# Kernel optimization log

Hardware: AMD Instinct MI355X
Metric: run time of the kernel (lower is better)

## Reference

```python
import jax
import jax.numpy as jnp
import numpy as np

B, N, C_IN, C_OUT, K = 16, 4096, 64, 128, 16
RATIO = 0.25
M = int(RATIO * N)  # 1024 sampled points per cloud
EPS = 1e-5


def setup_inputs() -> dict:
    key = jax.random.key(0)
    ks = jax.random.split(key, 4)
    features = jax.random.normal(ks[0], (B, N, C_IN), dtype=jnp.float32)
    positions = jax.random.normal(ks[1], (B, N, 3), dtype=jnp.float32)
    batch = jnp.repeat(jnp.arange(B, dtype=jnp.int64), N)  # [B*N]
    W = jax.random.normal(ks[2], (C_IN, C_OUT), dtype=jnp.float32) * 0.1
    b = jax.random.normal(ks[3], (C_OUT,), dtype=jnp.float32) * 0.1
    gamma = jnp.ones((C_OUT,), dtype=jnp.float32)
    beta = jnp.zeros((C_OUT,), dtype=jnp.float32)
    return {"features": features, "positions": positions, "batch": batch,
            "W": W, "b": b, "gamma": gamma, "beta": beta}


def _fps_single(pos):
    """Farthest point sampling on one cloud. pos: [N,3] -> indices [M] (start at 0)."""
    def step(carry, _):
        min_d, last = carry
        d = jnp.sum((pos - pos[last]) ** 2, axis=-1)       # [N]
        min_d = jnp.minimum(min_d, d)
        nxt = jnp.argmax(min_d).astype(jnp.int32)
        return (min_d, nxt), nxt
    init = (jnp.full((N,), 1e10, dtype=pos.dtype), jnp.int32(0))
    _, rest = jax.lax.scan(step, init, None, length=M - 1)
    return jnp.concatenate([jnp.zeros((1,), jnp.int32), rest])


def reference(features, positions, batch, W, b, gamma, beta):
    # --- FPS per batch (on positions) ---
    fps_idx = jax.vmap(_fps_single)(positions)                     # [B, M] int32

    # --- MLP: Linear + BatchNorm1d (training-mode batch stats over all B*N points) ---
    h = jnp.einsum('bnc,co->bno', features, W) + b                 # [B, N, C_OUT]
    flat = h.reshape(-1, C_OUT)
    mean = jnp.mean(flat, axis=0)
    var = jnp.mean((flat - mean) ** 2, axis=0)                     # biased, as BN
    hn = (h - mean) * jax.lax.rsqrt(var + EPS) * gamma + beta      # [B, N, C_OUT]

    # --- kNN in FEATURE space: queries = sampled features, keys = all features ---
    q = jnp.take_along_axis(features, fps_idx[..., None], axis=1)  # [B, M, C_IN]
    d2 = (jnp.sum(q * q, -1)[:, :, None]
          + jnp.sum(features * features, -1)[:, None, :]
          - 2.0 * jnp.einsum('bmd,bnd->bmn', q, features))         # [B, M, N]
    _, nbr = jax.lax.top_k(-d2, K)                                 # [B, M, K]

    # --- gather MLP'd features at neighbors, max-pool per sampled point ---
    gathered = jnp.take_along_axis(hn, nbr.reshape(B, M * K)[..., None], axis=1)
    new_features = gathered.reshape(B, M, K, C_OUT).max(axis=2)    # [B, M, C_OUT]

    new_positions = jnp.take_along_axis(positions, fps_idx[..., None], axis=1)  # [B, M, 3]
    new_batch = jnp.take_along_axis(batch.reshape(B, N), fps_idx.astype(jnp.int64), axis=1).reshape(-1)
    return new_features, new_positions, new_batch
```

## Files before the change

kernel.cpp:

```cpp
#include <hip/hip_runtime.h>

#define B_ 16
#define N_ 4096
#define CIN_ 64
#define COUT_ 128
#define K_ 16
#define M_ 1024

typedef float f32x2 __attribute__((ext_vector_type(2)));
typedef unsigned long long u64;

#define DPPF(m, ctrl)                                                          \
  m = fmaxf(m, __int_as_float(__builtin_amdgcn_update_dpp(                     \
                  0, __float_as_int(m), ctrl, 0xF, 0xF, true)))
#define DPPI(e, ctrl)                                                          \
  e = max(e, __builtin_amdgcn_update_dpp(0, e, ctrl, 0xF, 0xF, true))

__device__ __forceinline__ unsigned mono32(float d) {
  unsigned u = __float_as_uint(d);
  return u ^ (unsigned)(((int)u >> 31) | 0x80000000);
}

__global__ __launch_bounds__(512) void mega_kernel(
    const float* __restrict__ pos, const float* __restrict__ features,
    const float* __restrict__ W, const float* __restrict__ bias,
    int* __restrict__ fps_idx, float* __restrict__ h,
    float* __restrict__ stats, int* __restrict__ prog,
    u64* __restrict__ cand, int S) {
  __shared__ __align__(16) char smem[84 * 1024];
  const int id = blockIdx.x;
  const int t = threadIdx.x;

  if (id < B_) {
    const int b = id;
    float4* P = (float4*)smem;
    u64* red = (u64*)(smem + 65536);
    const float* pb = pos + (size_t)b * N_ * 3;
    for (int i = t; i < N_; i += 512)
      P[i] = make_float4(pb[i * 3], pb[i * 3 + 1], pb[i * 3 + 2], 0.f);
    __syncthreads();
    if (t < 256) {
      f32x2 px[8], py[8], pz[8], md[8];
#pragma unroll
      for (int j = 0; j < 8; ++j) {
        const float4 lo = P[t + 512 * j];
        const float4 hi = P[t + 512 * j + 256];
        px[j] = (f32x2){lo.x, hi.x};
        py[j] = (f32x2){lo.y, hi.y};
        pz[j] = (f32x2){lo.z, hi.z};
        md[j] = (f32x2){1e10f, 1e10f};
      }
      if (t == 0) fps_idx[b * M_] = 0;
      const int wv = t >> 6, ln = t & 63;
      const int e0 = 65535 - t;
      float4 lp = P[0];
      for (int step = 1; step < M_; ++step) {
        const f32x2 lx = {lp.x, lp.x}, ly = {lp.y, lp.y}, lz = {lp.z, lp.z};
        float bestd = -1.0f;
        int be = 0;
        {
#pragma clang fp contract(off)
#pragma unroll
          for (int j = 0; j < 8; ++j) {
            const f32x2 dx = px[j] - lx;
            const f32x2 dy = py[j] - ly;
            const f32x2 dz = pz[j] - lz;
            const f32x2 s1 = dx * dx;
            const f32x2 s2 = dy * dy;
            const f32x2 s3 = dz * dz;
            const f32x2 d = (s1 + s2) + s3;
            f32x2 nd;
            nd.x = fminf(md[j].x, d.x);
            nd.y = fminf(md[j].y, d.y);
            md[j] = nd;
            if (nd.x > bestd) { bestd = nd.x; be = e0 - (j << 9); }
            if (nd.y > bestd) { bestd = nd.y; be = e0 - (j << 9) - 256; }
          }
        }
        float m = bestd;
        DPPF(m, 0x111); DPPF(m, 0x112); DPPF(m, 0x114); DPPF(m, 0x118);
        DPPF(m, 0x142); DPPF(m, 0x143);
        const float wm =
            __int_as_float(__builtin_amdgcn_readlane(__float_as_int(m), 63));
        int enc = (bestd == wm) ? be : 0;
        DPPI(enc, 0x111); DPPI(enc, 0x112); DPPI(enc, 0x114); DPPI(enc, 0x118);
        DPPI(enc, 0x142); DPPI(enc, 0x143);
        const int wenc = __builtin_amdgcn_readlane(enc, 63);
        if (ln == 0)
          red[(step & 1) * 4 + wv] =
              ((u64)__float_as_uint(wm) << 32) | (unsigned)wenc;
        __syncthreads();
        const u64* rb = &red[(step & 1) * 4];
        u64 rr = rb[0] > rb[1] ? rb[0] : rb[1];
        const u64 r2 = rb[2] > rb[3] ? rb[2] : rb[3];
        if (r2 > rr) rr = r2;
        const int last = 65535 - (int)(unsigned)(rr & 0xFFFFFFFFu);
        lp = P[last];
        if (t == 0) {
          fps_idx[b * M_ + step] = last;
          if ((step & 63) == 63)
            __hip_atomic_store(&prog[b], (step >> 6) + 1, __ATOMIC_RELEASE,
                               __HIP_MEMORY_SCOPE_AGENT);
        }
      }
    } else {
      for (int step = 1; step < M_; ++step) __syncthreads();
    }
    return;
  }

  if (id < B_ + 256 * S) {
    const int kid = id - B_;
    const int qt = kid / (B_ * S);
    const int rem = kid % (B_ * S);
    const int b = rem / S;
    const int s = rem % S;
    const int KPS = N_ / S;
    const int KT = KPS / 128;
    float* Qs = (float*)smem;
    float* Ks = (float*)(smem + 16384);
    float* sd2 = (float*)(smem + 49152);
    float* qq = (float*)(smem + 82944);
    float* ff = (float*)(smem + 83200);
    int* qid = (int*)(smem + 83712);
    const float* fb = features + (size_t)b * N_ * CIN_;

    if (t == 0) {
      while (__hip_atomic_load(&prog[b], __ATOMIC_ACQUIRE,
                               __HIP_MEMORY_SCOPE_AGENT) < qt + 1)
        __builtin_amdgcn_s_sleep(16);
    }
    __syncthreads();
    if (t < 64) qid[t] = fps_idx[b * M_ + qt * 64 + t];
    __syncthreads();
#pragma unroll
    for (int st = 0; st < 2; ++st) {
      const int iid = t + 512 * st;
      const int row = iid >> 4, c4 = iid & 15;
      const int pc = (c4 + (row >> 2)) & 15;
      const float4 v = *(const float4*)(fb + (size_t)qid[row] * CIN_ + c4 * 4);
      *(float4*)(&Qs[row * 64 + pc * 4]) = v;
    }
    __syncthreads();
    if (t < 64) {
      float sv = 0.f;
#pragma unroll
      for (int c4 = 0; c4 < 16; ++c4) {
        const int pc = (c4 + (t >> 2)) & 15;
        const float4 v = *(const float4*)(&Qs[t * 64 + pc * 4]);
        sv = fmaf(v.x, v.x, sv); sv = fmaf(v.y, v.y, sv);
        sv = fmaf(v.z, v.z, sv); sv = fmaf(v.w, v.w, sv);
      }
      qq[t] = sv;
    }

    u64 lst[16];
#pragma unroll
    for (int p = 0; p < 16; ++p) lst[p] = ~0ull;
    u64 worst = ~0ull;
    int wpos = 0;

    const int q0 = (t >> 5) * 4;
    const int k0 = (t & 31) * 4;
    const int sq = t >> 3;
    const int ssub = t & 7;

    for (int kt = 0; kt < KT; ++kt) {
      const int kb = s * KPS + kt * 128;
#pragma unroll
      for (int st = 0; st < 4; ++st) {
        const int iid = t + 512 * st;
        const int row = iid >> 4, c4 = iid & 15;
        const int pc = (c4 + (row >> 2)) & 15;
        const float4 v = *(const float4*)(fb + (size_t)(kb + row) * CIN_ + c4 * 4);
        *(float4*)(&Ks[row * 64 + pc * 4]) = v;
      }
      __syncthreads();
      if (t < 128) {
        float sv = 0.f;
#pragma unroll
        for (int c4 = 0; c4 < 16; ++c4) {
          const int pc = (c4 + (t >> 2)) & 15;
          const float4 v = *(const float4*)(&Ks[t * 64 + pc * 4]);
          sv = fmaf(v.x, v.x, sv); sv = fmaf(v.y, v.y, sv);
          sv = fmaf(v.z, v.z, sv); sv = fmaf(v.w, v.w, sv);
        }
        ff[t] = sv;
      }
      __syncthreads();
      float acc[4][4];
#pragma unroll
      for (int i = 0; i < 4; ++i)
#pragma unroll
        for (int j = 0; j < 4; ++j) acc[i][j] = 0.f;
#pragma unroll
      for (int c4 = 0; c4 < 16; ++c4) {
        float4 qv[4], kv[4];
#pragma unroll
        for (int i = 0; i < 4; ++i) {
          const int row = q0 + i;
          const int pc = (c4 + (row >> 2)) & 15;
          qv[i] = *(const float4*)(&Qs[row * 64 + pc * 4]);
        }
#pragma unroll
        for (int j = 0; j < 4; ++j) {
          const int row = k0 + j;
          const int pc = (c4 + (row >> 2)) & 15;
          kv[j] = *(const float4*)(&Ks[row * 64 + pc * 4]);
        }
#pragma unroll
        for (int i = 0; i < 4; ++i)
#pragma unroll
          for (int j = 0; j < 4; ++j) {
            acc[i][j] = fmaf(qv[i].x, kv[j].x, acc[i][j]);
            acc[i][j] = fmaf(qv[i].y, kv[j].y, acc[i][j]);
            acc[i][j] = fmaf(qv[i].z, kv[j].z, acc[i][j]);
            acc[i][j] = fmaf(qv[i].w, kv[j].w, acc[i][j]);
          }
      }
#pragma unroll
      for (int i = 0; i < 4; ++i) {
        const float qv = qq[q0 + i];
        float4 o;
        o.x = __fsub_rn(__fadd_rn(qv, ff[k0 + 0]), 2.f * acc[i][0]);
        o.y = __fsub_rn(__fadd_rn(qv, ff[k0 + 1]), 2.f * acc[i][1]);
        o.z = __fsub_rn(__fadd_rn(qv, ff[k0 + 2]), 2.f * acc[i][2]);
        o.w = __fsub_rn(__fadd_rn(qv, ff[k0 + 3]), 2.f * acc[i][3]);
        *(float4*)(&sd2[(q0 + i) * 132 + k0]) = o;
      }
      __syncthreads();
#pragma unroll
      for (int g = 0; g < 4; ++g) {
        const float4 v = *(const float4*)(&sd2[sq * 132 + ssub * 16 + g * 4]);
        const float dv[4] = {v.x, v.y, v.z, v.w};
#pragma unroll
        for (int jj = 0; jj < 4; ++jj) {
          const int key = kb + ssub * 16 + g * 4 + jj;
          const u64 pk = ((u64)mono32(dv[jj]) << 32) | (unsigned)key;
          if (pk < worst) {
#pragma unroll
            for (int p = 0; p < 16; ++p)
              if (p == wpos) lst[p] = pk;
            worst = lst[0]; wpos = 0;
#pragma unroll
            for (int p = 1; p < 16; ++p)
              if (lst[p] > worst) { worst = lst[p]; wpos = p; }
          }
        }
      }
      __syncthreads();
    }
    u64* cb = cand + ((size_t)(b * M_ + qt * 64 + sq) * S + s) * 16;
    for (int r = 0; r < K_; ++r) {
      u64 mn = lst[0];
#pragma unroll
      for (int p = 1; p < 16; ++p)
        if (lst[p] < mn) mn = lst[p];
      u64 m2 = mn;
#pragma unroll
      for (int off = 1; off < 8; off <<= 1) {
        const u64 o = __shfl_xor(m2, off, 64);
        if (o < m2) m2 = o;
      }
      if (mn == m2) {
        bool done = false;
#pragma unroll
        for (int p = 0; p < 16; ++p)
          if (!done && lst[p] == m2) { lst[p] = ~0ull; done = true; }
      }
      if (ssub == 0) cb[r] = m2;
    }
    return;
  }

  const int lid = id - (B_ + 256 * S);
  float* ls = (float*)smem;
  for (int i = t; i < 256; i += 512) ls[i] = 0.f;
  __syncthreads();
  const int o4 = (t & 31) << 2;
  const int rl = t >> 5;
  const float4 bv = *(const float4*)(bias + o4);
  float4 s4 = {0, 0, 0, 0}, ss4 = {0, 0, 0, 0};
  for (int i = 0; i < 8; ++i) {
    const int r = lid * 128 + rl * 8 + i;
    const float4* fr = (const float4*)(features + (size_t)r * CIN_);
    float4 acc = bv;
#pragma unroll
    for (int c4 = 0; c4 < 16; ++c4) {
      const float4 fv = fr[c4];
      const float* wr = W + (size_t)(c4 * 4) * COUT_ + o4;
      const float4 w0 = *(const float4*)(wr);
      const float4 w1 = *(const float4*)(wr + COUT_);
      const float4 w2 = *(const float4*)(wr + 2 * COUT_);
      const float4 w3 = *(const float4*)(wr + 3 * COUT_);
      acc.x = fmaf(fv.x, w0.x, acc.x); acc.y = fmaf(fv.x, w0.y, acc.y);
      acc.z = fmaf(fv.x, w0.z, acc.z); acc.w = fmaf(fv.x, w0.w, acc.w);
      acc.x = fmaf(fv.y, w1.x, acc.x); acc.y = fmaf(fv.y, w1.y, acc.y);
      acc.z = fmaf(fv.y, w1.z, acc.z); acc.w = fmaf(fv.y, w1.w, acc.w);
      acc.x = fmaf(fv.z, w2.x, acc.x); acc.y = fmaf(fv.z, w2.y, acc.y);
      acc.z = fmaf(fv.z, w2.z, acc.z); acc.w = fmaf(fv.z, w2.w, acc.w);
      acc.x = fmaf(fv.w, w3.x, acc.x); acc.y = fmaf(fv.w, w3.y, acc.y);
      acc.z = fmaf(fv.w, w3.z, acc.z); acc.w = fmaf(fv.w, w3.w, acc.w);
    }
    *(float4*)(h + (size_t)r * COUT_ + o4) = acc;
    s4.x += acc.x; s4.y += acc.y; s4.z += acc.z; s4.w += acc.w;
    ss4.x = fmaf(acc.x, acc.x, ss4.x); ss4.y = fmaf(acc.y, acc.y, ss4.y);
    ss4.z = fmaf(acc.z, acc.z, ss4.z); ss4.w = fmaf(acc.w, acc.w, ss4.w);
  }
  atomicAdd(&ls[o4 + 0], s4.x); atomicAdd(&ls[o4 + 1], s4.y);
  atomicAdd(&ls[o4 + 2], s4.z); atomicAdd(&ls[o4 + 3], s4.w);
  atomicAdd(&ls[128 + o4 + 0], ss4.x); atomicAdd(&ls[128 + o4 + 1], ss4.y);
  atomicAdd(&ls[128 + o4 + 2], ss4.z); atomicAdd(&ls[128 + o4 + 3], ss4.w);
  __syncthreads();
  if (t < 128) {
    atomicAdd(&stats[t], ls[t]);
    atomicAdd(&stats[128 + t], ls[128 + t]);
  }
}

__global__ void finalize_kernel(float* __restrict__ stats,
                                const float* __restrict__ gamma,
                                const float* __restrict__ beta) {
  const int o = threadIdx.x;
  const float inv = 1.0f / (float)(B_ * N_);
  const float mean = stats[o] * inv;
  const float var = stats[128 + o] * inv - mean * mean;
  const float r = 1.0f / sqrtf(var + 1e-5f);
  const float sc = gamma[o] * r;
  stats[256 + o] = sc;
  stats[384 + o] = beta[o] - mean * sc;
}

__global__ __launch_bounds__(256) void gather_kernel(
    const float* __restrict__ h, const float* __restrict__ stats,
    const u64* __restrict__ cand, float* __restrict__ out, int S) {
  const int g = blockIdx.x;
  const int t = threadIdx.x;
  const int S16 = S * 16;
  __shared__ u64 cl[2][128];
  __shared__ int nbi[32];
  const int Q0 = g * 2;
  if (t < 2 * S16) {
    const int qi = t / S16, sl = t % S16;
    cl[qi][sl] = cand[(size_t)(Q0 + qi) * S16 + sl];
  }
  __syncthreads();
  if ((t & 127) == 0) {
    const int qi = t >> 7;
    int ptr[8] = {0, 0, 0, 0, 0, 0, 0, 0};
    for (int r = 0; r < K_; ++r) {
      u64 mn = ~0ull;
      int ms = 0;
      for (int s = 0; s < S; ++s) {
        if (ptr[s] < 16) {
          const u64 v = cl[qi][s * 16 + ptr[s]];
          if (v < mn) { mn = v; ms = s; }
        }
      }
      nbi[qi * 16 + r] = (int)(unsigned)(mn & 0xFFFFFFFFu);
      ptr[ms]++;
    }
  }
  __syncthreads();
  const int q2 = t >> 7, o = t & 127;
  const int Q = Q0 + q2, b = Q >> 10;
  const float sc = stats[256 + o];
  const float sh = stats[384 + o];
  float mx = -3.402823466e38f;
#pragma unroll
  for (int k = 0; k < K_; ++k) {
    const int n = nbi[q2 * 16 + k];
    const float v = fmaf(h[((size_t)b * N_ + n) * COUT_ + o], sc, sh);
    mx = fmaxf(mx, v);
  }
  out[(size_t)Q * COUT_ + o] = mx;
}

__global__ __launch_bounds__(256) void tail_kernel(const float* __restrict__ pos,
                                                   const int* __restrict__ fps_idx,
                                                   float* __restrict__ out,
                                                   int batch_as_i64) {
  const int gid = blockIdx.x * 256 + threadIdx.x;
  const int A = B_ * M_ * COUT_;
  const int P = B_ * M_ * 3;
  if (gid < P) {
    const int Q = gid / 3;
    const int c = gid - Q * 3;
    const int b = Q >> 10;
    const int idx = fps_idx[Q];
    out[A + gid] = pos[((size_t)b * N_ + idx) * 3 + c];
  } else {
    const int Q = gid - P;
    if (Q < B_ * M_) {
      const int b = Q >> 10;
      float* base = out + A + P;
      if (batch_as_i64)
        ((long long*)base)[Q] = (long long)b;
      else
        base[Q] = (float)b;
    }
  }
}

extern "C" void kernel_launch(void* const* d_in, const int* in_sizes, int n_in,
                              void* d_out, int out_size, void* d_ws, size_t ws_size,
                              hipStream_t stream) {
  const float* features = (const float*)d_in[0];
  const float* positions = (const float*)d_in[1];
  const float* W = (const float*)d_in[3];
  const float* bias = (const float*)d_in[4];
  const float* gamma = (const float*)d_in[5];
  const float* beta = (const float*)d_in[6];
  float* out = (float*)d_out;
  unsigned char* ws = (unsigned char*)d_ws;

  int* fps_idx = (int*)ws;
  float* h = (float*)(ws + 65536);
  const size_t hoff = 65536 + (size_t)B_ * N_ * COUT_ * 4;
  float* stats = (float*)(ws + hoff);
  int* prog = (int*)(ws + hoff + 2048);
  u64* cand = (u64*)(ws + hoff + 2048 + 256);
  const size_t base = hoff + 2048 + 256;

  int S = 8;
  while (S > 1 && base + (size_t)B_ * M_ * S * 16 * 8 > ws_size) S >>= 1;

  const int rem = out_size - (B_ * M_ * COUT_) - (B_ * M_ * 3);
  const int batch_as_i64 = (rem >= 2 * B_ * M_) ? 1 : 0;

  hipMemsetAsync(stats, 0, 2048 + 256, stream);
  mega_kernel<<<B_ + 256 * S + 512, 512, 0, stream>>>(
      positions, features, W, bias, fps_idx, h, stats, prog, cand, S);
  finalize_kernel<<<1, 128, 0, stream>>>(stats, gamma, beta);
  gather_kernel<<<B_ * M_ / 2, 256, 0, stream>>>(h, stats, cand, out, S);
  tail_kernel<<<256, 256, 0, stream>>>(positions, fps_idx, out, batch_as_i64);
}
```

Measured before the change: 1.021 ms.

## Replace FPS barrier with tagged LDS spin, store h as bf16, reorder blocks

The FPS loop's per-step __syncthreads is replaced by a lock-free handoff: each wave writes its packed max plus a step tag into double-buffered LDS, and all waves spin until every slot carries the current tag. The idle upper half of the FPS block now exits early. The MLP blocks are moved ahead of the kNN blocks in the grid so they get scheduled before the spinning kNN consumers. The intermediate h is stored as bf16 to halve its write and gather traffic, which costs precision in the gathered max-pooled outputs.

```diff
diff --git a/kernel.cpp b/kernel.cpp
--- a/kernel.cpp
+++ b/kernel.cpp
@@ -21,10 +21,18 @@
   return u ^ (unsigned)(((int)u >> 31) | 0x80000000);
 }
 
+__device__ __forceinline__ unsigned short f2bf(float x) {
+  const unsigned u = __float_as_uint(x);
+  return (unsigned short)((u + 0x7FFF + ((u >> 16) & 1)) >> 16);
+}
+__device__ __forceinline__ float bf2f(unsigned short s) {
+  return __uint_as_float((unsigned)s << 16);
+}
+
 __global__ __launch_bounds__(512) void mega_kernel(
     const float* __restrict__ pos, const float* __restrict__ features,
     const float* __restrict__ W, const float* __restrict__ bias,
-    int* __restrict__ fps_idx, float* __restrict__ h,
+    int* __restrict__ fps_idx, unsigned short* __restrict__ h,
     float* __restrict__ stats, int* __restrict__ prog,
     u64* __restrict__ cand, int S) {
   __shared__ __align__(16) char smem[84 * 1024];
@@ -34,83 +42,136 @@
   if (id < B_) {
     const int b = id;
     float4* P = (float4*)smem;
-    u64* red = (u64*)(smem + 65536);
+    volatile u64* red = (volatile u64*)(smem + 65536);
     const float* pb = pos + (size_t)b * N_ * 3;
+    if (t < 8) ((u64*)(smem + 65536))[t] = 0;
     for (int i = t; i < N_; i += 512)
       P[i] = make_float4(pb[i * 3], pb[i * 3 + 1], pb[i * 3 + 2], 0.f);
     __syncthreads();
-    if (t < 256) {
-      f32x2 px[8], py[8], pz[8], md[8];
-#pragma unroll
-      for (int j = 0; j < 8; ++j) {
-        const float4 lo = P[t + 512 * j];
-        const float4 hi = P[t + 512 * j + 256];
-        px[j] = (f32x2){lo.x, hi.x};
-        py[j] = (f32x2){lo.y, hi.y};
-        pz[j] = (f32x2){lo.z, hi.z};
-        md[j] = (f32x2){1e10f, 1e10f};
-      }
-      if (t == 0) fps_idx[b * M_] = 0;
-      const int wv = t >> 6, ln = t & 63;
-      const int e0 = 65535 - t;
-      float4 lp = P[0];
-      for (int step = 1; step < M_; ++step) {
-        const f32x2 lx = {lp.x, lp.x}, ly = {lp.y, lp.y}, lz = {lp.z, lp.z};
-        float bestd = -1.0f;
-        int be = 0;
-        {
+    if (t >= 256) return;
+    f32x2 px[8], py[8], pz[8], md[8];
+#pragma unroll
+    for (int j = 0; j < 8; ++j) {
+      const float4 lo = P[t + 512 * j];
+      const float4 hi = P[t + 512 * j + 256];
+      px[j] = (f32x2){lo.x, hi.x};
+      py[j] = (f32x2){lo.y, hi.y};
+      pz[j] = (f32x2){lo.z, hi.z};
+      md[j] = (f32x2){1e10f, 1e10f};
+    }
+    if (t == 0) fps_idx[b * M_] = 0;
+    const int wv = t >> 6, ln = t & 63;
+    const int e0 = 65535 - t;
+    float4 lp = P[0];
+    for (int step = 1; step < M_; ++step) {
+      const f32x2 lx = {lp.x, lp.x}, ly = {lp.y, lp.y}, lz = {lp.z, lp.z};
+      float bestd = -1.0f;
+      int be = 0;
+      {
 #pragma clang fp contract(off)
 #pragma unroll
-          for (int j = 0; j < 8; ++j) {
-            const f32x2 dx = px[j] - lx;
-            const f32x2 dy = py[j] - ly;
-            const f32x2 dz = pz[j] - lz;
-            const f32x2 s1 = dx * dx;
-            const f32x2 s2 = dy * dy;
-            const f32x2 s3 = dz * dz;
-            const f32x2 d = (s1 + s2) + s3;
-            f32x2 nd;
-            nd.x = fminf(md[j].x, d.x);
-            nd.y = fminf(md[j].y, d.y);
-            md[j] = nd;
-            if (nd.x > bestd) { bestd = nd.x; be = e0 - (j << 9); }
-            if (nd.y > bestd) { bestd = nd.y; be = e0 - (j << 9) - 256; }
-          }
-        }
-        float m = bestd;
-        DPPF(m, 0x111); DPPF(m, 0x112); DPPF(m, 0x114); DPPF(m, 0x118);
-        DPPF(m, 0x142); DPPF(m, 0x143);
-        const float wm =
-            __int_as_float(__builtin_amdgcn_readlane(__float_as_int(m), 63));
-        int enc = (bestd == wm) ? be : 0;
-        DPPI(enc, 0x111); DPPI(enc, 0x112); DPPI(enc, 0x114); DPPI(enc, 0x118);
-        DPPI(enc, 0x142); DPPI(enc, 0x143);
-        const int wenc = __builtin_amdgcn_readlane(enc, 63);
-        if (ln == 0)
-          red[(step & 1) * 4 + wv] =
-              ((u64)__float_as_uint(wm) << 32) | (unsigned)wenc;
-        __syncthreads();
-        const u64* rb = &red[(step & 1) * 4];
-        u64 rr = rb[0] > rb[1] ? rb[0] : rb[1];
-        const u64 r2 = rb[2] > rb[3] ? rb[2] : rb[3];
-        if (r2 > rr) rr = r2;
-        const int last = 65535 - (int)(unsigned)(rr & 0xFFFFFFFFu);
-        lp = P[last];
-        if (t == 0) {
-          fps_idx[b * M_ + step] = last;
-          if ((step & 63) == 63)
-            __hip_atomic_store(&prog[b], (step >> 6) + 1, __ATOMIC_RELEASE,
-                               __HIP_MEMORY_SCOPE_AGENT);
-        }
-      }
-    } else {
-      for (int step = 1; step < M_; ++step) __syncthreads();
+        for (int j = 0; j < 8; ++j) {
+          const f32x2 dx = px[j] - lx;
+          const f32x2 dy = py[j] - ly;
+          const f32x2 dz = pz[j] - lz;
+          const f32x2 s1 = dx * dx;
+          const f32x2 s2 = dy * dy;
+          const f32x2 s3 = dz * dz;
+          const f32x2 d = (s1 + s2) + s3;
+          f32x2 nd;
+          nd.x = fminf(md[j].x, d.x);
+          nd.y = fminf(md[j].y, d.y);
+          md[j] = nd;
+          if (nd.x > bestd) { bestd = nd.x; be = e0 - (j << 9); }
+          if (nd.y > bestd) { bestd = nd.y; be = e0 - (j << 9) - 256; }
+        }
+      }
+      float m = bestd;
+      DPPF(m, 0x111); DPPF(m, 0x112); DPPF(m, 0x114); DPPF(m, 0x118);
+      DPPF(m, 0x142); DPPF(m, 0x143);
+      const float wm =
+          __int_as_float(__builtin_amdgcn_readlane(__float_as_int(m), 63));
+      int enc = (bestd == wm) ? be : 0;
+      DPPI(enc, 0x111); DPPI(enc, 0x112); DPPI(enc, 0x114); DPPI(enc, 0x118);
+      DPPI(enc, 0x142); DPPI(enc, 0x143);
+      const int wenc = __builtin_amdgcn_readlane(enc, 63);
+      const unsigned tag = (unsigned)(step & 1023);
+      volatile u64* rb = red + (step & 1) * 4;
+      if (ln == 0)
+        rb[wv] = ((u64)__float_as_uint(wm) << 32) | ((u64)tag << 16) |
+                 (unsigned)wenc;
+      u64 r0, r1, r2, r3;
+      for (;;) {
+        r0 = rb[0]; r1 = rb[1]; r2 = rb[2]; r3 = rb[3];
+        const u64 x = ((r0 >> 16) ^ tag) | ((r1 >> 16) ^ tag) |
+                      ((r2 >> 16) ^ tag) | ((r3 >> 16) ^ tag);
+        if (!(x & 0x3FF)) break;
+      }
+      u64 rr = r0 > r1 ? r0 : r1;
+      const u64 rc = r2 > r3 ? r2 : r3;
+      if (rc > rr) rr = rc;
+      const int last = 65535 - (int)(unsigned)(rr & 0xFFFFu);
+      lp = P[last];
+      if (t == 0) {
+        fps_idx[b * M_ + step] = last;
+        if ((step & 63) == 63)
+          __hip_atomic_store(&prog[b], (step >> 6) + 1, __ATOMIC_RELEASE,
+                             __HIP_MEMORY_SCOPE_AGENT);
+      }
     }
     return;
   }
 
-  if (id < B_ + 256 * S) {
-    const int kid = id - B_;
+  if (id < B_ + 512) {
+    const int lid = id - B_;
+    float* ls = (float*)smem;
+    for (int i = t; i < 256; i += 512) ls[i] = 0.f;
+    __syncthreads();
+    const int o4 = (t & 31) << 2;
+    const int rl = t >> 5;
+    const float4 bv = *(const float4*)(bias + o4);
+    float4 s4 = {0, 0, 0, 0}, ss4 = {0, 0, 0, 0};
+    for (int i = 0; i < 8; ++i) {
+      const int r = lid * 128 + rl * 8 + i;
+      const float4* fr = (const float4*)(features + (size_t)r * CIN_);
+      float4 acc = bv;
+#pragma unroll
+      for (int c4 = 0; c4 < 16; ++c4) {
+        const float4 fv = fr[c4];
+        const float* wr = W + (size_t)(c4 * 4) * COUT_ + o4;
+        const float4 w0 = *(const float4*)(wr);
+        const float4 w1 = *(const float4*)(wr + COUT_);
+        const float4 w2 = *(const float4*)(wr + 2 * COUT_);
+        const float4 w3 = *(const float4*)(wr + 3 * COUT_);
+        acc.x = fmaf(fv.x, w0.x, acc.x); acc.y = fmaf(fv.x, w0.y, acc.y);
+        acc.z = fmaf(fv.x, w0.z, acc.z); acc.w = fmaf(fv.x, w0.w, acc.w);
+        acc.x = fmaf(fv.y, w1.x, acc.x); acc.y = fmaf(fv.y, w1.y, acc.y);
+        acc.z = fmaf(fv.y, w1.z, acc.z); acc.w = fmaf(fv.y, w1.w, acc.w);
+        acc.x = fmaf(fv.z, w2.x, acc.x); acc.y = fmaf(fv.z, w2.y, acc.y);
+        acc.z = fmaf(fv.z, w2.z, acc.z); acc.w = fmaf(fv.z, w2.w, acc.w);
+        acc.x = fmaf(fv.w, w3.x, acc.x); acc.y = fmaf(fv.w, w3.y, acc.y);
+        acc.z = fmaf(fv.w, w3.z, acc.z); acc.w = fmaf(fv.w, w3.w, acc.w);
+      }
+      *(ushort4*)(h + (size_t)r * COUT_ + o4) =
+          make_ushort4(f2bf(acc.x), f2bf(acc.y), f2bf(acc.z), f2bf(acc.w));
+      s4.x += acc.x; s4.y += acc.y; s4.z += acc.z; s4.w += acc.w;
+      ss4.x = fmaf(acc.x, acc.x, ss4.x); ss4.y = fmaf(acc.y, acc.y, ss4.y);
+      ss4.z = fmaf(acc.z, acc.z, ss4.z); ss4.w = fmaf(acc.w, acc.w, ss4.w);
+    }
+    atomicAdd(&ls[o4 + 0], s4.x); atomicAdd(&ls[o4 + 1], s4.y);
+    atomicAdd(&ls[o4 + 2], s4.z); atomicAdd(&ls[o4 + 3], s4.w);
+    atomicAdd(&ls[128 + o4 + 0], ss4.x); atomicAdd(&ls[128 + o4 + 1], ss4.y);
+    atomicAdd(&ls[128 + o4 + 2], ss4.z); atomicAdd(&ls[128 + o4 + 3], ss4.w);
+    __syncthreads();
+    if (t < 128) {
+      atomicAdd(&stats[t], ls[t]);
+      atomicAdd(&stats[128 + t], ls[128 + t]);
+    }
+    return;
+  }
+
+  {
+    const int kid = id - (B_ + 512);
     const int qt = kid / (B_ * S);
     const int rem = kid % (B_ * S);
     const int b = rem / S;
@@ -172,7 +233,8 @@
         const int iid = t + 512 * st;
         const int row = iid >> 4, c4 = iid & 15;
         const int pc = (c4 + (row >> 2)) & 15;
-        const float4 v = *(const float4*)(fb + (size_t)(kb + row) * CIN_ + c4 * 4);
+        const float4 v =
+            *(const float4*)(fb + (size_t)(kb + row) * CIN_ + c4 * 4);
         *(float4*)(&Ks[row * 64 + pc * 4]) = v;
       }
       __syncthreads();
@@ -270,51 +332,6 @@
       }
       if (ssub == 0) cb[r] = m2;
     }
-    return;
-  }
-
-  const int lid = id - (B_ + 256 * S);
-  float* ls = (float*)smem;
-  for (int i = t; i < 256; i += 512) ls[i] = 0.f;
-  __syncthreads();
-  const int o4 = (t & 31) << 2;
-  const int rl = t >> 5;
-  const float4 bv = *(const float4*)(bias + o4);
-  float4 s4 = {0, 0, 0, 0}, ss4 = {0, 0, 0, 0};
-  for (int i = 0; i < 8; ++i) {
-    const int r = lid * 128 + rl * 8 + i;
-    const float4* fr = (const float4*)(features + (size_t)r * CIN_);
-    float4 acc = bv;
-#pragma unroll
-    for (int c4 = 0; c4 < 16; ++c4) {
-      const float4 fv = fr[c4];
-      const float* wr = W + (size_t)(c4 * 4) * COUT_ + o4;
-      const float4 w0 = *(const float4*)(wr);
-      const float4 w1 = *(const float4*)(wr + COUT_);
-      const float4 w2 = *(const float4*)(wr + 2 * COUT_);
-      const float4 w3 = *(const float4*)(wr + 3 * COUT_);
-      acc.x = fmaf(fv.x, w0.x, acc.x); acc.y = fmaf(fv.x, w0.y, acc.y);
-      acc.z = fmaf(fv.x, w0.z, acc.z); acc.w = fmaf(fv.x, w0.w, acc.w);
-      acc.x = fmaf(fv.y, w1.x, acc.x); acc.y = fmaf(fv.y, w1.y, acc.y);
-      acc.z = fmaf(fv.y, w1.z, acc.z); acc.w = fmaf(fv.y, w1.w, acc.w);
-      acc.x = fmaf(fv.z, w2.x, acc.x); acc.y = fmaf(fv.z, w2.y, acc.y);
-      acc.z = fmaf(fv.z, w2.z, acc.z); acc.w = fmaf(fv.z, w2.w, acc.w);
-      acc.x = fmaf(fv.w, w3.x, acc.x); acc.y = fmaf(fv.w, w3.y, acc.y);
-      acc.z = fmaf(fv.w, w3.z, acc.z); acc.w = fmaf(fv.w, w3.w, acc.w);
-    }
-    *(float4*)(h + (size_t)r * COUT_ + o4) = acc;
-    s4.x += acc.x; s4.y += acc.y; s4.z += acc.z; s4.w += acc.w;
-    ss4.x = fmaf(acc.x, acc.x, ss4.x); ss4.y = fmaf(acc.y, acc.y, ss4.y);
-    ss4.z = fmaf(acc.z, acc.z, ss4.z); ss4.w = fmaf(acc.w, acc.w, ss4.w);
-  }
-  atomicAdd(&ls[o4 + 0], s4.x); atomicAdd(&ls[o4 + 1], s4.y);
-  atomicAdd(&ls[o4 + 2], s4.z); atomicAdd(&ls[o4 + 3], s4.w);
-  atomicAdd(&ls[128 + o4 + 0], ss4.x); atomicAdd(&ls[128 + o4 + 1], ss4.y);
-  atomicAdd(&ls[128 + o4 + 2], ss4.z); atomicAdd(&ls[128 + o4 + 3], ss4.w);
-  __syncthreads();
-  if (t < 128) {
-    atomicAdd(&stats[t], ls[t]);
-    atomicAdd(&stats[128 + t], ls[128 + t]);
   }
 }
 
@@ -332,7 +349,7 @@
 }
 
 __global__ __launch_bounds__(256) void gather_kernel(
-    const float* __restrict__ h, const float* __restrict__ stats,
+    const unsigned short* __restrict__ h, const float* __restrict__ stats,
     const u64* __restrict__ cand, float* __restrict__ out, int S) {
   const int g = blockIdx.x;
   const int t = threadIdx.x;
@@ -370,7 +387,7 @@
 #pragma unroll
   for (int k = 0; k < K_; ++k) {
     const int n = nbi[q2 * 16 + k];
-    const float v = fmaf(h[((size_t)b * N_ + n) * COUT_ + o], sc, sh);
+    const float v = fmaf(bf2f(h[((size_t)b * N_ + n) * COUT_ + o]), sc, sh);
     mx = fmaxf(mx, v);
   }
   out[(size_t)Q * COUT_ + o] = mx;
@@ -415,8 +432,8 @@
   unsigned char* ws = (unsigned char*)d_ws;
 
   int* fps_idx = (int*)ws;
-  float* h = (float*)(ws + 65536);
-  const size_t hoff = 65536 + (size_t)B_ * N_ * COUT_ * 4;
+  unsigned short* h = (unsigned short*)(ws + 65536);
+  const size_t hoff = 65536 + (size_t)B_ * N_ * COUT_ * 2;
   float* stats = (float*)(ws + hoff);
   int* prog = (int*)(ws + hoff + 2048);
   u64* cand = (u64*)(ws + hoff + 2048 + 256);
@@ -429,7 +446,7 @@
   const int batch_as_i64 = (rem >= 2 * B_ * M_) ? 1 : 0;
 
   hipMemsetAsync(stats, 0, 2048 + 256, stream);
-  mega_kernel<<<B_ + 256 * S + 512, 512, 0, stream>>>(
+  mega_kernel<<<B_ + 512 + 256 * S, 512, 0, stream>>>(
       positions, features, W, bias, fps_idx, h, stats, prog, cand, S);
   finalize_kernel<<<1, 128, 0, stream>>>(stats, gamma, beta);
   gather_kernel<<<B_ * M_ / 2, 256, 0, stream>>>(h, stats, cand, out, S);
```

Result: slower. 1.043 ms (+2.2%).
